# Performance work log

Hardware: AMD Instinct MI355X
Metric: run time of the kernel (lower is better)

The kernel has to match this reference:

```python
import jax, jax.numpy as jnp
import numpy as np

L = 8      # num_hidden_layers
J = 3      # num_gnn_layers
N = 2000   # num nodes (<=2000 so prune=False)
E = 32000  # num edges
R = 64     # num relations
HID = 1024 # hidden_dim
G = 128    # gnn_dim
H = 8      # num_gnn_heads
DH = G // H          # 16 per-head dim
P = 10               # pre_seq_len
KV = 8               # plm_num_kv_heads
OUT = HID // 32 * KV # out_ft_dim = 256
B = 16               # batch (h.shape[0])


def setup_inputs() -> dict:
    key = jax.random.key(0)
    ks = jax.random.split(key, 24)
    f = lambda k, s: (jax.random.normal(k, s, dtype=jnp.float32) * 0.05)
    ri = lambda k, s, hi: jax.random.randint(k, s, 0, hi, dtype=jnp.int32)
    return {
        'nft': f(ks[0], (L, N, HID)),
        'rft': f(ks[1], (L, R, HID)),
        'importances': jax.random.normal(ks[2], (N,), dtype=jnp.float32),
        'tg_w': f(ks[3], (L, HID, G)),
        'tg_b': f(ks[4], (L, G)),
        'path_w': f(ks[5], (L, J, 3 * G, G)),
        'path_b': f(ks[6], (L, J, G)),
        'attn1_w': f(ks[7], (L, J, G, H)),
        'attn2_p': f(ks[8], (L, J, H, DH)),
        'trans_w': f(ks[9], (L, G, 2 * OUT)),
        'trans_b': f(ks[10], (L, 2 * OUT)),
        'lamda': jnp.zeros((L - 1,), dtype=jnp.float32),
        'edge_src': ri(ks[11], (E,), N),
        'edge_dst': ri(ks[12], (E,), N),
        'edge_label': ri(ks[13], (E,), R),
        'h': ri(ks[14], (B,), N),
        't': ri(ks[15], (B,), N),
    }


def _gat(x, eft, src, dst, Wp, bp, Wa1, a2p):
    # x: [N, G], eft: [E, G]
    ns = x[src]                       # [E, G] gather src node feats
    ne = x[dst]                       # [E, G] gather dst node feats
    epaths = (jnp.concatenate([ns, eft, ne], axis=-1) @ Wp + bp)
    epaths = epaths.reshape(E, H, DH)           # per-edge multi-head features
    a1 = ns @ Wa1                               # [E, H]
    a2 = jnp.einsum('ehd,hd->eh', epaths, a2p)  # [E, H]
    a = jax.nn.leaky_relu(a1 + a2)              # slope 0.01, matches torch default
    # edge softmax grouped by destination node
    amax = jax.ops.segment_max(a, dst, num_segments=N)
    ex = jnp.exp(a - amax[dst])
    ssum = jax.ops.segment_sum(ex, dst, num_segments=N)
    attn = ex / ssum[dst]                       # [E, H]
    msg = epaths * attn[..., None]              # [E, H, DH]
    agg = jax.ops.segment_sum(msg, dst, num_segments=N)  # [N, H, DH]
    return jax.nn.relu(agg.reshape(N, G) + x)


def reference(nft, rft, importances, tg_w, tg_b, path_w, path_b, attn1_w,
              attn2_p, trans_w, trans_b, lamda, edge_src, edge_dst,
              edge_label, h, t):
    bsz = h.shape[0]
    # topk indices of node importances (prune=False path)
    _, imp_idx = jax.lax.top_k(importances, P)
    pkv = []
    for i in range(L):
        x = nft[i] @ tg_w[i] + tg_b[i]                       # [N, G]
        # linear-then-gather == gather-then-linear (same math, less traffic)
        rel = rft[i] @ tg_w[i] + tg_b[i]                     # [R, G]
        gnn_eft = rel[edge_label]                            # [E, G]
        for j in range(J):
            x = _gat(x, gnn_eft, edge_src, edge_dst,
                     path_w[i, j], path_b[i, j], attn1_w[i, j], attn2_p[i, j])
        past_x = x
        if i > 0:
            s = jax.nn.sigmoid(lamda[i - 1] / 0.1)
            x = s * x + (1.0 - s) * past_x   # past_x == x (as in source)
        prefix = x[imp_idx]                                  # [P, G]
        pk = jnp.tanh(prefix) @ trans_w[i] + trans_b[i]      # [P, 2*OUT]
        pk = jnp.broadcast_to(pk[None], (bsz, P, 2 * OUT))
        pk = pk.reshape(bsz, P, 2, KV, OUT // KV).transpose(2, 0, 3, 1, 4)
        pkv.append(pk)
    return jnp.stack(pkv)   # [L, 2, B, KV, P, OUT//KV]
```

## Files before the change

kernel.cpp:

```cpp
#include <hip/hip_runtime.h>
#include <hip/hip_bf16.h>
#include <math.h>

#define L_    8
#define J_    3
#define N_    2000
#define E_    32000
#define R_    64
#define HID_  1024
#define G_    128
#define H_    8
#define DH_   16
#define P_    10
#define KV_   8
#define OUT2_ 512
#define B_    16
#define ROWS_ 2064
#define CAP_  64

typedef float f32x4 __attribute__((ext_vector_type(4)));
typedef short s16x8 __attribute__((ext_vector_type(8)));

__device__ __forceinline__ void cvt_split1(float v, short& h, short& l) {
    unsigned u = __float_as_uint(v);
    h = (short)(u >> 16);
    float rem = v - __uint_as_float(u & 0xffff0000u);
    l = (short)(__float_as_uint(rem) >> 16);
}

__device__ __forceinline__ void cvt_split8(const float* v, s16x8& h, s16x8& l) {
    #pragma unroll
    for (int i = 0; i < 8; ++i) {
        unsigned u = __float_as_uint(v[i]);
        h[i] = (short)(u >> 16);
        float rem = v[i] - __uint_as_float(u & 0xffff0000u);
        l[i] = (short)(__float_as_uint(rem) >> 16);
    }
}

__device__ __forceinline__ void cvt_split8v(float4 a, float4 b, s16x8& h, s16x8& l) {
    short hh, ll;
    cvt_split1(a.x, hh, ll); h[0] = hh; l[0] = ll;
    cvt_split1(a.y, hh, ll); h[1] = hh; l[1] = ll;
    cvt_split1(a.z, hh, ll); h[2] = hh; l[2] = ll;
    cvt_split1(a.w, hh, ll); h[3] = hh; l[3] = ll;
    cvt_split1(b.x, hh, ll); h[4] = hh; l[4] = ll;
    cvt_split1(b.y, hh, ll); h[5] = hh; l[5] = ll;
    cvt_split1(b.z, hh, ll); h[6] = hh; l[6] = ll;
    cvt_split1(b.w, hh, ll); h[7] = hh; l[7] = ll;
}


__device__ __forceinline__ void place_body(int b, const int* __restrict__ dst,
                                           const int* __restrict__ src,
                                           const int* __restrict__ lab,
                                           int* __restrict__ cur,
                                           int2* __restrict__ sl) {
    int e = b * 128 + threadIdx.x;
    if (e < E_) {
        int n = dst[e];
        int slot = atomicAdd(&cur[n], 1);
        sl[n * CAP_ + slot] = make_int2(src[e], lab[e]);
    }
}

__device__ __forceinline__ void topk_body(const float* __restrict__ imp,
                                          int* __restrict__ idx_out, char* pool) {
    float* sv = (float*)pool;
    float* rv = (float*)(pool + 8192);
    int*   ri = (int*)(pool + 8704);
    int t = threadIdx.x;
    for (int i = t; i < N_; i += 128) sv[i] = imp[i];
    __syncthreads();
    for (int k = 0; k < P_; ++k) {
        float bv = -INFINITY; int bi = N_;
        for (int i = t; i < N_; i += 128) {
            float v = sv[i];
            if (v > bv || (v == bv && i < bi)) { bv = v; bi = i; }
        }
        rv[t] = bv; ri[t] = bi;
        __syncthreads();
        for (int s = 64; s > 0; s >>= 1) {
            if (t < s) {
                float v = rv[t + s]; int i2 = ri[t + s];
                if (v > rv[t] || (v == rv[t] && i2 < ri[t])) { rv[t] = v; ri[t] = i2; }
            }
            __syncthreads();
        }
        if (t == 0) { idx_out[k] = ri[0]; sv[ri[0]] = -INFINITY; }
        __syncthreads();
    }
}

__device__ __forceinline__ void psplit_body(int l, int j, int halfc, int st,
                                            const float* __restrict__ path_w,
                                            short* __restrict__ Ppk) {
    int lj = l * J_ + j;
    int col = threadIdx.x;
    int c0 = halfc ? 256 : 0;
    size_t base = (((size_t)lj * 2 + halfc) * 4 + st) * 2;
    #pragma unroll
    for (int khalf = 0; khalf < 2; ++khalf) {
        const float* src = path_w + (size_t)lj * 384 * G_
                         + (size_t)(c0 + st * 32 + khalf * 16) * G_ + col;
        short* dh = Ppk + (base + 0) * 4096 + (khalf * 128 + col) * 16;
        short* dl = Ppk + (base + 1) * 4096 + (khalf * 128 + col) * 16;
        #pragma unroll
        for (int kk = 0; kk < 16; ++kk) {
            short h, l2;
            cvt_split1(src[(size_t)kk * G_], h, l2);
            dh[kk] = h; dl[kk] = l2;
        }
    }
}

__device__ __forceinline__ void prep_body(int combo, int q,
                                          const float* __restrict__ path_w,
                                          const float* __restrict__ path_b,
                                          const float* __restrict__ attn1_w,
                                          const float* __restrict__ attn2_p,
                                          float* __restrict__ wPR,
                                          short* __restrict__ PPk,
                                          float* __restrict__ bA) {
    int j = combo / L_;
    int l = combo % L_;
    int t = threadIdx.x;
    size_t wb = (size_t)((l * J_ + j) * 384) * G_;
    size_t ob = (size_t)(j * L_ + l);
    const float* a2 = attn2_p + (size_t)(l * J_ + j) * G_;
    short* pph = PPk + (ob * 2 + 0) * 2048;
    short* ppl = PPk + (ob * 2 + 1) * 2048;
    #pragma unroll
    for (int h2 = 0; h2 < 2; ++h2) {
        int i = q * 256 + h2 * 128 + t;
        int k = i >> 3, h = i & 7;
        const float* a2h = a2 + h * DH_;
        float s1 = 0.f, s2 = 0.f, s3 = 0.f;
        for (int d = 0; d < DH_; ++d) {
            float av = a2h[d];
            int c = h * DH_ + d;
            s1 += path_w[wb + (size_t)k * G_ + c] * av;
            s3 += path_w[wb + (size_t)(128 + k) * G_ + c] * av;
            s2 += path_w[wb + (size_t)(256 + k) * G_ + c] * av;
        }
        s1 += attn1_w[((size_t)(l * J_ + j) * G_ + k) * H_ + h];
        short h1, l1, hh2, l2;
        cvt_split1(s1, h1, l1);
        cvt_split1(s2, hh2, l2);
        pph[h * 128 + k] = h1;        ppl[h * 128 + k] = l1;
        pph[(8 + h) * 128 + k] = hh2; ppl[(8 + h) * 128 + k] = l2;
        wPR[ob * H_ * G_ + h * G_ + k] = s3;
    }
    if (q == 0 && t < H_) {
        float s = 0.f;
        const float* a2h = a2 + t * DH_;
        const float* pb = path_b + (size_t)(l * J_ + j) * G_ + t * DH_;
        for (int d = 0; d < DH_; ++d) s += pb[d] * a2h[d];
        bA[ob * H_ + t] = s;
    }
}

__global__ __launch_bounds__(256) void k_pre0(
    const float* __restrict__ tg_w, short* __restrict__ WpkB,
    int* __restrict__ cur) {
    int b = blockIdx.x;
    if (b == 256) {
        for (int i = threadIdx.x; i < N_; i += 256) cur[i] = 0;
        return;
    }
    int layer = b & 7, gst = b >> 3;
    int tid = threadIdx.x;
    int col = tid & 127, khalf = tid >> 7;
    const float* src = tg_w + ((size_t)layer * HID_ + gst * 32 + khalf * 16) * G_ + col;
    short* dh = WpkB + ((size_t)(layer * 32 + gst) * 2 + 0) * 4096 + col * 32 + khalf * 16;
    short* dl = WpkB + ((size_t)(layer * 32 + gst) * 2 + 1) * 4096 + col * 32 + khalf * 16;
    #pragma unroll
    for (int kk = 0; kk < 16; ++kk) {
        short h, l;
        cvt_split1(src[(size_t)kk * G_], h, l);
        dh[kk] = h; dl[kk] = l;
    }
}

__global__ __launch_bounds__(128, 2) void k_pre3(
    const float* __restrict__ nft, const float* __restrict__ rft,
    const short* __restrict__ WpkB, const float* __restrict__ tg_b,
    float* __restrict__ x0, float* __restrict__ rel,
    const int* __restrict__ edst, const int* __restrict__ esrc,
    const int* __restrict__ elab, const float* __restrict__ imp,
    const float* __restrict__ path_w, const float* __restrict__ path_b,
    const float* __restrict__ attn1_w, const float* __restrict__ attn2_p,
    int* __restrict__ cur, int2* __restrict__ csr_sl, int* __restrict__ imp_idx,
    short* __restrict__ Ppk, float* __restrict__ wPR,
    short* __restrict__ PPk, float* __restrict__ bA) {
    __shared__ alignas(16) char POOL3[12288];
    int b = blockIdx.x;
    if (b >= 520) {
        int w = b - 520;
        if (w < 250) { place_body(w, edst, esrc, elab, cur, csr_sl); return; }
        if (w == 250) { topk_body(imp, imp_idx, POOL3); return; }
        if (w < 443) {
            int v = w - 251;
            int l = v & 7, m = v >> 3;
            int j = m % 3, hs = m / 3;
            psplit_body(l, j, hs >> 2, hs & 3, path_w, Ppk);
            return;
        }
        {
            int v = w - 443;
            prep_body(v >> 2, v & 3, path_w, path_b, attn1_w, attn2_p, wPR, PPk, bA);
            return;
        }
    }

    const int layer = b & 7;
    const int rg = b >> 3;
    const int row0 = rg * 32;
    const int tid = threadIdx.x;
    const int lane = tid & 63, wv = tid >> 6;
    const int lr = lane & 15, kg = lane >> 4;

    char* ldsb = POOL3;

    const float* gsrc0;
    const float* gsrc1;
    {
        int swz = ((lane & 7) ^ (lane >> 3)) << 2;
        int rl0 = wv * 16 + (lane >> 3);
        int rl1 = rl0 + 8;
        int g0 = row0 + rl0; if (g0 > ROWS_ - 1) g0 = ROWS_ - 1;
        int g1 = row0 + rl1; if (g1 > ROWS_ - 1) g1 = ROWS_ - 1;
        gsrc0 = ((g0 < N_) ? nft + ((size_t)layer * N_ + g0) * HID_
                           : rft + ((size_t)layer * R_ + (g0 - N_)) * HID_) + swz;
        gsrc1 = ((g1 < N_) ? nft + ((size_t)layer * N_ + g1) * HID_
                           : rft + ((size_t)layer * R_ + (g1 - N_)) * HID_) + swz;
    }
    const short* WB = WpkB + (size_t)layer * 262144 + ((wv * 64 + lr) * 32 + kg * 8);

    f32x4 zero = {0.f, 0.f, 0.f, 0.f};
    f32x4 acc[2][4];
    #pragma unroll
    for (int i = 0; i < 2; ++i)
        #pragma unroll
        for (int n = 0; n < 4; ++n) acc[i][n] = zero;

    s16x8 bs[2][4][2];

#define LDA(WR, GST) do { \
    char* lb_ = ldsb + (WR) * 4096 + wv * 2048; \
    __builtin_amdgcn_global_load_lds( \
        (const __attribute__((address_space(1))) void*)(gsrc0 + (GST) * 32), \
        (__attribute__((address_space(3))) void*)(lb_), 16, 0, 0); \
    __builtin_amdgcn_global_load_lds( \
        (const __attribute__((address_space(1))) void*)(gsrc1 + (GST) * 32), \
        (__attribute__((address_space(3))) void*)(lb_ + 1024), 16, 0, 0); \
} while (0)

#define LDB(SL, GST) do { \
    const short* bp_ = WB + (size_t)(GST) * 8192; \
    _Pragma("unroll") \
    for (int n_ = 0; n_ < 4; ++n_) { \
        bs[SL][n_][0] = *(const s16x8*)(bp_ + n_ * 512); \
        bs[SL][n_][1] = *(const s16x8*)(bp_ + n_ * 512 + 4096); \
    } \
} while (0)

#define COMP(CUR, SL) do { \
    const int o1_ = (kg * 32) ^ ((lr & 7) << 4); \
    _Pragma("unroll") \
    for (int mf_ = 0; mf_ < 2; ++mf_) { \
        const char* ap_ = ldsb + (CUR) * 4096 + (mf_ * 16 + lr) * 128; \
        float4 av0_ = *(const float4*)(ap_ + o1_); \
        float4 av1_ = *(const float4*)(ap_ + (o1_ ^ 16)); \
        s16x8 ah_, al_; \
        cvt_split8v(av0_, av1_, ah_, al_); \
        _Pragma("unroll") \
        for (int n_ = 0; n_ < 4; ++n_) { \
            acc[mf_][n_] = __builtin_amdgcn_mfma_f32_16x16x32_bf16(ah_, bs[SL][n_][0], acc[mf_][n_], 0, 0, 0); \
            acc[mf_][n_] = __builtin_amdgcn_mfma_f32_16x16x32_bf16(ah_, bs[SL][n_][1], acc[mf_][n_], 0, 0, 0); \
            acc[mf_][n_] = __builtin_amdgcn_mfma_f32_16x16x32_bf16(al_, bs[SL][n_][0], acc[mf_][n_], 0, 0, 0); \
        } \
    } \
} while (0)

#define TGITER(ST, CUR, WR, SL, SLN) do { \
    LDB(SLN, (ST) + 1); \
    LDA(WR, (ST) + 2); \
    asm volatile("s_waitcnt vmcnt(12)" ::: "memory"); \
    __builtin_amdgcn_s_barrier(); \
    COMP(CUR, SL); \
    __builtin_amdgcn_s_barrier(); \
} while (0)

    LDA(0, 0);
    LDA(1, 1);
    LDB(0, 0);
    for (int st = 0; st < 30; st += 6) {
        TGITER(st + 0, 0, 2, 0, 1);
        TGITER(st + 1, 1, 0, 1, 0);
        TGITER(st + 2, 2, 1, 0, 1);
        TGITER(st + 3, 0, 2, 1, 0);
        TGITER(st + 4, 1, 0, 0, 1);
        TGITER(st + 5, 2, 1, 1, 0);
    }
    LDB(1, 31);
    asm volatile("s_waitcnt vmcnt(10)" ::: "memory");
    __builtin_amdgcn_s_barrier();
    COMP(0, 0);
    asm volatile("s_waitcnt vmcnt(0)" ::: "memory");
    __builtin_amdgcn_s_barrier();
    COMP(1, 1);
#undef LDA
#undef LDB
#undef COMP
#undef TGITER

    #pragma unroll
    for (int n = 0; n < 4; ++n) {
        int col = wv * 64 + n * 16 + lr;
        float bias = tg_b[layer * G_ + col];
        #pragma unroll
        for (int mf = 0; mf < 2; ++mf) {
            #pragma unroll
            for (int rgi = 0; rgi < 4; ++rgi) {
                int row = row0 + mf * 16 + kg * 4 + rgi;
                if (row >= ROWS_) continue;
                float v = acc[mf][n][rgi] + bias;
                if (row < N_) x0[((size_t)layer * N_ + row) * G_ + col] = v;
                else          rel[((size_t)layer * R_ + (row - N_)) * G_ + col] = v;
            }
        }
    }
}

__device__ __forceinline__ void rel_body(
    int blk, char* pool,
    const float* __restrict__ rel, const float* __restrict__ path_w,
    const float* __restrict__ wPR, float* __restrict__ Rl, float* __restrict__ PR) {
    float (*At)[132] = (float(*)[132])pool;
    float (*Wt)[132] = (float(*)[132])(pool + 16896);
    const int tid = threadIdx.x;
    const int halfb = blk & 1;
    const int t2 = blk >> 1;
    const int l = t2 % L_;
    const int j = t2 / L_;
    const int row0 = halfb * 32;
    const size_t ob = (size_t)(j * L_ + l);
    {
        int ar = tid >> 3, aq2 = tid & 7;
        const float* asrc = rel + ((size_t)l * R_ + row0 + ar) * G_ + aq2 * 16;
        float4 a0 = ((const float4*)asrc)[0], a1 = ((const float4*)asrc)[1];
        float4 a2 = ((const float4*)asrc)[2], a3 = ((const float4*)asrc)[3];
        *(float4*)&At[ar][aq2 * 16]      = a0;
        *(float4*)&At[ar][aq2 * 16 + 4]  = a1;
        *(float4*)&At[ar][aq2 * 16 + 8]  = a2;
        *(float4*)&At[ar][aq2 * 16 + 12] = a3;
    }
    const size_t wb = (size_t)((l * J_ + j) * 384) * G_;
    const int wrow = tid >> 3, wq = tid & 7;
    float4 rW0, rW1, rW2, rW3;
    auto loadW = [&](int kt) {
        const float* src = path_w + wb + (size_t)(128 + kt * 32 + wrow) * G_ + wq * 16;
        rW0 = ((const float4*)src)[0]; rW1 = ((const float4*)src)[1];
        rW2 = ((const float4*)src)[2]; rW3 = ((const float4*)src)[3];
    };
    const int tr = tid >> 4;
    const int tc = tid & 15;
    float4 acc[2][2];
    acc[0][0] = make_float4(0, 0, 0, 0); acc[0][1] = make_float4(0, 0, 0, 0);
    acc[1][0] = make_float4(0, 0, 0, 0); acc[1][1] = make_float4(0, 0, 0, 0);
    loadW(0);
    for (int wt = 0; wt < 4; ++wt) {
        __syncthreads();
        *(float4*)&Wt[wrow][wq * 16]      = rW0;
        *(float4*)&Wt[wrow][wq * 16 + 4]  = rW1;
        *(float4*)&Wt[wrow][wq * 16 + 8]  = rW2;
        *(float4*)&Wt[wrow][wq * 16 + 12] = rW3;
        __syncthreads();
        if (wt + 1 < 4) loadW(wt + 1);
        #pragma unroll
        for (int kk = 0; kk < 32; ++kk) {
            float4 w0 = *(const float4*)&Wt[kk][tc * 4];
            float4 w1 = *(const float4*)&Wt[kk][64 + tc * 4];
            float a0 = At[tr * 2][wt * 32 + kk];
            float a1 = At[tr * 2 + 1][wt * 32 + kk];
            acc[0][0].x += a0 * w0.x; acc[0][0].y += a0 * w0.y;
            acc[0][0].z += a0 * w0.z; acc[0][0].w += a0 * w0.w;
            acc[0][1].x += a0 * w1.x; acc[0][1].y += a0 * w1.y;
            acc[0][1].z += a0 * w1.z; acc[0][1].w += a0 * w1.w;
            acc[1][0].x += a1 * w0.x; acc[1][0].y += a1 * w0.y;
            acc[1][0].z += a1 * w0.z; acc[1][0].w += a1 * w0.w;
            acc[1][1].x += a1 * w1.x; acc[1][1].y += a1 * w1.y;
            acc[1][1].z += a1 * w1.z; acc[1][1].w += a1 * w1.w;
        }
    }
    #pragma unroll
    for (int r2 = 0; r2 < 2; ++r2) {
        int row = row0 + tr * 2 + r2;
        float* dst = Rl + (ob * R_ + row) * G_;
        *(float4*)(dst + tc * 4) = acc[r2][0];
        *(float4*)(dst + 64 + tc * 4) = acc[r2][1];
    }
    {
        int prow = tid >> 3, ph = tid & 7;
        const float* wp = wPR + (ob * H_ + ph) * G_;
        float s = 0.f;
        for (int k = 0; k < G_; ++k) s += At[prow][k] * wp[k];
        PR[(ob * R_ + row0 + prow) * H_ + ph] = s;
    }
}

__global__ __launch_bounds__(256) void k_proj2(
    const float* __restrict__ xcur, const short* __restrict__ Ppk,
    const short* __restrict__ PPkj, const float* __restrict__ bAj,
    const float* __restrict__ path_b, int j,
    float* __restrict__ Xs, float* __restrict__ XdB,
    float* __restrict__ PS, float* __restrict__ PDb,
    const float* __restrict__ rel, const float* __restrict__ path_w,
    const float* __restrict__ wPR, float* __restrict__ Rl, float* __restrict__ PR) {
    __shared__ alignas(16) char POOL[39424];
    if (blockIdx.x >= 512) { rel_body(blockIdx.x - 512, POOL, rel, path_w, wPR, Rl, PR); return; }
    short (*Ah)[40]   = (short(*)[40])(POOL);
    short (*Al)[40]   = (short(*)[40])(POOL + 5120);
    short (*Wh)[40]   = (short(*)[40])(POOL + 10240);
    short (*Wl)[40]   = (short(*)[40])(POOL + 20480);
    short (*PPh)[136] = (short(*)[136])(POOL + 30720);
    short (*PPl)[136] = (short(*)[136])(POOL + 35072);
    const int tid = threadIdx.x;
    const int layer = blockIdx.x & 7;
    const int rest = blockIdx.x >> 3;
    const int halfb = rest & 1;
    const int rg = rest >> 1;
    const int row0 = rg * 64;

    const int arow = tid >> 2, aq = tid & 3;
    int gra = row0 + arow; if (gra >= N_) gra = N_ - 1;
    const float* asrc = xcur + ((size_t)layer * N_ + gra) * G_;
    const int wcol = tid & 127, wkh = tid >> 7;

    const int lane = tid & 63, wv = tid >> 6;
    const int lr = lane & 15, lk = (lane >> 4) * 8;

    if (!halfb) {
        int col = tid >> 4, koff = (tid & 15) * 8;
        s16x8 vh = *(const s16x8*)(PPkj + ((size_t)layer * 2 + 0) * 2048 + tid * 8);
        s16x8 vl = *(const s16x8*)(PPkj + ((size_t)layer * 2 + 1) * 2048 + tid * 8);
        *(s16x8*)&PPh[col][koff] = vh;
        *(s16x8*)&PPl[col][koff] = vl;
    }

    f32x4 zero = {0.f, 0.f, 0.f, 0.f};
    f32x4 acc[4][2];
    f32x4 acc_pp[2];
    #pragma unroll
    for (int i = 0; i < 4; ++i) { acc[i][0] = zero; acc[i][1] = zero; }
    acc_pp[0] = zero; acc_pp[1] = zero;

    float aa[8];
    s16x8 wh0, wh1, wl0, wl1;
    const size_t pbase = (((size_t)(layer * J_ + j) * 2 + halfb) * 4) * 2;
    auto ldG = [&](int st) {
        int kk0 = st * 32;
        *(float4*)&aa[0] = *(const float4*)(asrc + kk0 + aq * 8);
        *(float4*)&aa[4] = *(const float4*)(asrc + kk0 + aq * 8 + 4);
        const s16x8* ph = (const s16x8*)(Ppk + (pbase + (size_t)st * 2 + 0) * 4096 + tid * 16);
        const s16x8* pl = (const s16x8*)(Ppk + (pbase + (size_t)st * 2 + 1) * 4096 + tid * 16);
        wh0 = ph[0]; wh1 = ph[1];
        wl0 = pl[0]; wl1 = pl[1];
    };
    ldG(0);
    for (int st = 0; st < 4; ++st) {
        __syncthreads();
        {
            s16x8 h, l; cvt_split8(aa, h, l);
            *(s16x8*)&Ah[arow][aq * 8] = h;
            *(s16x8*)&Al[arow][aq * 8] = l;
            *(s16x8*)&Wh[wcol][wkh * 16]     = wh0;
            *(s16x8*)&Wh[wcol][wkh * 16 + 8] = wh1;
            *(s16x8*)&Wl[wcol][wkh * 16]     = wl0;
            *(s16x8*)&Wl[wcol][wkh * 16 + 8] = wl1;
        }
        __syncthreads();
        if (st + 1 < 4) ldG(st + 1);
        s16x8 bh[2], bl[2];
        #pragma unroll
        for (int c = 0; c < 2; ++c) {
            int col = wv * 32 + c * 16 + lr;
            bh[c] = *(s16x8*)&Wh[col][lk];
            bl[c] = *(s16x8*)&Wl[col][lk];
        }
        s16x8 ppb_h, ppb_l;
        if (!halfb) {
            ppb_h = *(s16x8*)&PPh[lr][st * 32 + lk];
            ppb_l = *(s16x8*)&PPl[lr][st * 32 + lk];
        }
        #pragma unroll
        for (int mf = 0; mf < 4; ++mf) {
            s16x8 ah = *(s16x8*)&Ah[mf * 16 + lr][lk];
            s16x8 al = *(s16x8*)&Al[mf * 16 + lr][lk];
            #pragma unroll
            for (int c = 0; c < 2; ++c) {
                acc[mf][c] = __builtin_amdgcn_mfma_f32_16x16x32_bf16(ah, bh[c], acc[mf][c], 0, 0, 0);
                acc[mf][c] = __builtin_amdgcn_mfma_f32_16x16x32_bf16(ah, bl[c], acc[mf][c], 0, 0, 0);
                acc[mf][c] = __builtin_amdgcn_mfma_f32_16x16x32_bf16(al, bh[c], acc[mf][c], 0, 0, 0);
            }
            if (!halfb && (mf >> 1) == wv) {
                int i = mf & 1;
                acc_pp[i] = __builtin_amdgcn_mfma_f32_16x16x32_bf16(ah, ppb_h, acc_pp[i], 0, 0, 0);
                acc_pp[i] = __builtin_amdgcn_mfma_f32_16x16x32_bf16(ah, ppb_l, acc_pp[i], 0, 0, 0);
                acc_pp[i] = __builtin_amdgcn_mfma_f32_16x16x32_bf16(al, ppb_h, acc_pp[i], 0, 0, 0);
            }
        }
    }
    const float* pb = path_b + (size_t)(layer * J_ + j) * G_;
    float* outp = halfb ? XdB : Xs;
    const int rbase = (lane >> 4) * 4;
    #pragma unroll
    for (int mf = 0; mf < 4; ++mf) {
        #pragma unroll
        for (int c = 0; c < 2; ++c) {
            int col = wv * 32 + c * 16 + lr;
            float bias = halfb ? pb[col] : 0.f;
            #pragma unroll
            for (int rgi = 0; rgi < 4; ++rgi) {
                int row = row0 + mf * 16 + rbase + rgi;
                if (row < N_) outp[((size_t)layer * N_ + row) * G_ + col] = acc[mf][c][rgi] + bias;
            }
        }
    }
    if (!halfb) {
        #pragma unroll
        for (int i = 0; i < 2; ++i) {
            int mf = wv * 2 + i;
            #pragma unroll
            for (int rgi = 0; rgi < 4; ++rgi) {
                int row = row0 + mf * 16 + rbase + rgi;
                if (row >= N_) continue;
                float val = acc_pp[i][rgi];
                if (lr < 8) PS[((size_t)layer * N_ + row) * H_ + lr] = val;
                else        PDb[((size_t)layer * N_ + row) * H_ + (lr - 8)] = val + bAj[layer * H_ + (lr - 8)];
            }
        }
    }
}

__global__ __launch_bounds__(256) void k_node(
    const float* __restrict__ xcur, const float* __restrict__ Xs,
    const float* __restrict__ XdB, const float* __restrict__ Rlj,
    const float* __restrict__ PS, const float* __restrict__ PDb,
    const float* __restrict__ PRj,
    const int* __restrict__ cnt, const int2* __restrict__ csr_sl,
    float* __restrict__ xnext) {
    int l = blockIdx.x & 7;
    int n = (blockIdx.x >> 3) * 4 + (threadIdx.x >> 6);
    int lane = threadIdx.x & 63;
    int o0 = n * CAP_, o1 = o0 + cnt[n];
    const float* xr = xcur + ((size_t)l * N_ + n) * G_;
    float xv0 = xr[lane], xv1 = xr[lane + 64];
    float xd0 = XdB[((size_t)l * N_ + n) * G_ + lane];
    float xd1 = XdB[((size_t)l * N_ + n) * G_ + lane + 64];
    float out0, out1;
    if (o1 == o0) {
        out0 = fmaxf(xv0, 0.f);
        out1 = fmaxf(xv1, 0.f);
    } else {
        const int h0 = lane >> 4, h1 = h0 + 4;
        const float pd0 = PDb[((size_t)l * N_ + n) * H_ + h0];
        const float pd1 = PDb[((size_t)l * N_ + n) * H_ + h1];
        const float* PSl = PS + (size_t)l * N_ * H_;
        const float* PRl = PRj + (size_t)l * R_ * H_;
        const float* Xsl = Xs + (size_t)l * N_ * G_;
        const float* Rll = Rlj + (size_t)l * R_ * G_;
        float acc0 = 0.f, acc1 = 0.f, sum0 = 0.f, sum1 = 0.f;
        #pragma unroll 2
        for (int k = o0; k < o1; ++k) {
            int2 sl = csr_sl[k];
            float lg0 = PSl[sl.x * H_ + h0] + PRl[sl.y * H_ + h0] + pd0;
            float lg1 = PSl[sl.x * H_ + h1] + PRl[sl.y * H_ + h1] + pd1;
            lg0 = (lg0 >= 0.f) ? lg0 : 0.01f * lg0;
            lg1 = (lg1 >= 0.f) ? lg1 : 0.01f * lg1;
            float e0 = __expf(lg0), e1 = __expf(lg1);
            float v0 = Xsl[(size_t)sl.x * G_ + lane]      + Rll[(size_t)sl.y * G_ + lane];
            float v1 = Xsl[(size_t)sl.x * G_ + lane + 64] + Rll[(size_t)sl.y * G_ + lane + 64];
            acc0 += e0 * v0; sum0 += e0;
            acc1 += e1 * v1; sum1 += e1;
        }
        out0 = fmaxf(acc0 / sum0 + xd0 + xv0, 0.f);
        out1 = fmaxf(acc1 / sum1 + xd1 + xv1, 0.f);
    }
    float* dst = xnext + ((size_t)l * N_ + n) * G_;
    dst[lane] = out0;
    dst[lane + 64] = out1;
}

__global__ __launch_bounds__(256) void k_out(
    const float* __restrict__ xfin, const int* __restrict__ imp_idx,
    const float* __restrict__ trans_w, const float* __restrict__ trans_b,
    float* __restrict__ out) {
    int blk = blockIdx.x;
    int layer = blk / (P_ * 2);
    int rem = blk % (P_ * 2);
    int p = rem >> 1;
    int half = rem & 1;
    __shared__ float th[G_];
    int t = threadIdx.x;
    int row = imp_idx[p];
    if (t < G_) th[t] = tanhf(xfin[((size_t)layer * N_ + row) * G_ + t]);
    __syncthreads();
    int c = half * 256 + t;
    float s = trans_b[layer * OUT2_ + c];
    const float* W = trans_w + (size_t)layer * G_ * OUT2_ + c;
    #pragma unroll 4
    for (int k = 0; k < G_; ++k) s += th[k] * W[(size_t)k * OUT2_];
    int c2 = c >> 8, kv = (c >> 5) & 7, oo = c & 31;
    for (int b = 0; b < B_; ++b) {
        out[(((((size_t)layer * 2 + c2) * B_ + b) * KV_ + kv) * P_ + p) * 32 + oo] = s;
    }
}

extern "C" void kernel_launch(void* const* d_in, const int* in_sizes, int n_in,
                              void* d_out, int out_size, void* d_ws, size_t ws_size,
                              hipStream_t stream) {
    const float* nft     = (const float*)d_in[0];
    const float* rft     = (const float*)d_in[1];
    const float* imp     = (const float*)d_in[2];
    const float* tg_w    = (const float*)d_in[3];
    const float* tg_b    = (const float*)d_in[4];
    const float* path_w  = (const float*)d_in[5];
    const float* path_b  = (const float*)d_in[6];
    const float* attn1_w = (const float*)d_in[7];
    const float* attn2_p = (const float*)d_in[8];
    const float* trans_w = (const float*)d_in[9];
    const float* trans_b = (const float*)d_in[10];
    const int* esrc = (const int*)d_in[12];
    const int* edst = (const int*)d_in[13];
    const int* elab = (const int*)d_in[14];
    float* out = (float*)d_out;

    char* w = (char*)d_ws;
    size_t off = 0;
    auto alloc = [&](size_t bytes) {
        void* p = w + off;
        off += (bytes + 255) & ~(size_t)255;
        return p;
    };
    float* x0      = (float*)alloc((size_t)L_ * N_ * G_ * 4);
    float* x1      = (float*)alloc((size_t)L_ * N_ * G_ * 4);
    float* rel     = (float*)alloc((size_t)L_ * R_ * G_ * 4);
    float* Xs      = (float*)alloc((size_t)L_ * N_ * G_ * 4);
    float* XdB     = (float*)alloc((size_t)L_ * N_ * G_ * 4);
    float* Rl      = (float*)alloc((size_t)J_ * L_ * R_ * G_ * 4);
    float* PS      = (float*)alloc((size_t)L_ * N_ * H_ * 4);
    float* PDb     = (float*)alloc((size_t)L_ * N_ * H_ * 4);
    float* PR      = (float*)alloc((size_t)J_ * L_ * R_ * H_ * 4);
    float* wPR     = (float*)alloc((size_t)J_ * L_ * H_ * G_ * 4);
    float* bA      = (float*)alloc((size_t)J_ * L_ * H_ * 4);
    short* Wpk     = (short*)alloc((size_t)L_ * 32 * 2 * 4096 * 2);
    short* Ppk     = (short*)alloc((size_t)L_ * J_ * 2 * 4 * 2 * 4096 * 2);
    short* PPk     = (short*)alloc((size_t)J_ * L_ * 2 * 2048 * 2);
    int*   cur     = (int*)alloc(N_ * 4);
    int2*  csr_sl  = (int2*)alloc((size_t)N_ * CAP_ * 8);
    int*   imp_idx = (int*)alloc(P_ * 4);

    k_pre0<<<257, 256, 0, stream>>>(tg_w, Wpk, cur);
    k_pre3<<<520 + 250 + 1 + 192 + 96, 128, 0, stream>>>(
        nft, rft, Wpk, tg_b, x0, rel,
        edst, esrc, elab, imp, path_w, path_b, attn1_w, attn2_p,
        cur, csr_sl, imp_idx, Ppk, wPR, PPk, bA);

    float* xc = x0;
    float* xn = x1;
    for (int j = 0; j < J_; ++j) {
        int grid = (j == 0) ? (512 + J_ * L_ * 2) : 512;
        k_proj2<<<grid, 256, 0, stream>>>(
            xc, Ppk, PPk + (size_t)j * L_ * 2 * 2048, bA + (size_t)j * L_ * H_,
            path_b, j, Xs, XdB, PS, PDb,
            rel, path_w, wPR, Rl, PR);
        k_node<<<L_ * 500, 256, 0, stream>>>(
            xc, Xs, XdB, Rl + (size_t)j * L_ * R_ * G_, PS, PDb,
            PR + (size_t)j * L_ * R_ * H_,
            cur, csr_sl, xn);
        float* tmp = xc; xc = xn; xn = tmp;
    }
    k_out<<<L_ * P_ * 2, 256, 0, stream>>>(xc, imp_idx, trans_w, trans_b, out);
}
```

Before: 182.3 us.

## Halve row tile of node-feature GEMM to double block count

Each block of the pre-projection GEMM now covers 16 rows instead of 32, so the grid grows from 520 to 1032 tiles. Each block issues a single A-row load per stage, keeps one accumulator set, and uses half the LDS. Launch bounds rise to allow more resident blocks, and the vmcnt waits are retuned to the smaller load count. The aim is more parallelism and better latency hiding on this memory-bound stage. In exchange, every B-weight fragment is now loaded twice as often across blocks, since each block reuses it over fewer rows.

```diff
diff --git a/kernel.cpp b/kernel.cpp
--- a/kernel.cpp
+++ b/kernel.cpp
@@ -17,6 +17,7 @@
 #define B_    16
 #define ROWS_ 2064
 #define CAP_  64
+#define GB_   1032
 
 typedef float f32x4 __attribute__((ext_vector_type(4)));
 typedef short s16x8 __attribute__((ext_vector_type(8)));
@@ -182,7 +183,7 @@
     }
 }
 
-__global__ __launch_bounds__(128, 2) void k_pre3(
+__global__ __launch_bounds__(128, 4) void k_pre3(
     const float* __restrict__ nft, const float* __restrict__ rft,
     const short* __restrict__ WpkB, const float* __restrict__ tg_b,
     float* __restrict__ x0, float* __restrict__ rel,
@@ -195,8 +196,8 @@
     short* __restrict__ PPk, float* __restrict__ bA) {
     __shared__ alignas(16) char POOL3[12288];
     int b = blockIdx.x;
-    if (b >= 520) {
-        int w = b - 520;
+    if (b >= GB_) {
+        int w = b - GB_;
         if (w < 250) { place_body(w, edst, esrc, elab, cur, csr_sl); return; }
         if (w == 250) { topk_body(imp, imp_idx, POOL3); return; }
         if (w < 443) {
@@ -215,7 +216,7 @@
 
     const int layer = b & 7;
     const int rg = b >> 3;
-    const int row0 = rg * 32;
+    const int row0 = rg * 16;
     const int tid = threadIdx.x;
     const int lane = tid & 63, wv = tid >> 6;
     const int lr = lane & 15, kg = lane >> 4;
@@ -223,37 +224,27 @@
     char* ldsb = POOL3;
 
     const float* gsrc0;
-    const float* gsrc1;
     {
         int swz = ((lane & 7) ^ (lane >> 3)) << 2;
-        int rl0 = wv * 16 + (lane >> 3);
-        int rl1 = rl0 + 8;
-        int g0 = row0 + rl0; if (g0 > ROWS_ - 1) g0 = ROWS_ - 1;
-        int g1 = row0 + rl1; if (g1 > ROWS_ - 1) g1 = ROWS_ - 1;
-        gsrc0 = ((g0 < N_) ? nft + ((size_t)layer * N_ + g0) * HID_
-                           : rft + ((size_t)layer * R_ + (g0 - N_)) * HID_) + swz;
-        gsrc1 = ((g1 < N_) ? nft + ((size_t)layer * N_ + g1) * HID_
-                           : rft + ((size_t)layer * R_ + (g1 - N_)) * HID_) + swz;
+        int rb = row0 + wv * 8 + (lane >> 3);
+        if (rb > ROWS_ - 1) rb = ROWS_ - 1;
+        gsrc0 = ((rb < N_) ? nft + ((size_t)layer * N_ + rb) * HID_
+                           : rft + ((size_t)layer * R_ + (rb - N_)) * HID_) + swz;
     }
     const short* WB = WpkB + (size_t)layer * 262144 + ((wv * 64 + lr) * 32 + kg * 8);
 
     f32x4 zero = {0.f, 0.f, 0.f, 0.f};
-    f32x4 acc[2][4];
-    #pragma unroll
-    for (int i = 0; i < 2; ++i)
-        #pragma unroll
-        for (int n = 0; n < 4; ++n) acc[i][n] = zero;
+    f32x4 acc4[4];
+    #pragma unroll
+    for (int n = 0; n < 4; ++n) acc4[n] = zero;
 
     s16x8 bs[2][4][2];
 
 #define LDA(WR, GST) do { \
-    char* lb_ = ldsb + (WR) * 4096 + wv * 2048; \
+    char* lb_ = ldsb + (WR) * 2048 + wv * 1024; \
     __builtin_amdgcn_global_load_lds( \
         (const __attribute__((address_space(1))) void*)(gsrc0 + (GST) * 32), \
         (__attribute__((address_space(3))) void*)(lb_), 16, 0, 0); \
-    __builtin_amdgcn_global_load_lds( \
-        (const __attribute__((address_space(1))) void*)(gsrc1 + (GST) * 32), \
-        (__attribute__((address_space(3))) void*)(lb_ + 1024), 16, 0, 0); \
 } while (0)
 
 #define LDB(SL, GST) do { \
@@ -267,26 +258,23 @@
 
 #define COMP(CUR, SL) do { \
     const int o1_ = (kg * 32) ^ ((lr & 7) << 4); \
+    const char* ap_ = ldsb + (CUR) * 2048 + lr * 128; \
+    float4 av0_ = *(const float4*)(ap_ + o1_); \
+    float4 av1_ = *(const float4*)(ap_ + (o1_ ^ 16)); \
+    s16x8 ah_, al_; \
+    cvt_split8v(av0_, av1_, ah_, al_); \
     _Pragma("unroll") \
-    for (int mf_ = 0; mf_ < 2; ++mf_) { \
-        const char* ap_ = ldsb + (CUR) * 4096 + (mf_ * 16 + lr) * 128; \
-        float4 av0_ = *(const float4*)(ap_ + o1_); \
-        float4 av1_ = *(const float4*)(ap_ + (o1_ ^ 16)); \
-        s16x8 ah_, al_; \
-        cvt_split8v(av0_, av1_, ah_, al_); \
-        _Pragma("unroll") \
-        for (int n_ = 0; n_ < 4; ++n_) { \
-            acc[mf_][n_] = __builtin_amdgcn_mfma_f32_16x16x32_bf16(ah_, bs[SL][n_][0], acc[mf_][n_], 0, 0, 0); \
-            acc[mf_][n_] = __builtin_amdgcn_mfma_f32_16x16x32_bf16(ah_, bs[SL][n_][1], acc[mf_][n_], 0, 0, 0); \
-            acc[mf_][n_] = __builtin_amdgcn_mfma_f32_16x16x32_bf16(al_, bs[SL][n_][0], acc[mf_][n_], 0, 0, 0); \
-        } \
+    for (int n_ = 0; n_ < 4; ++n_) { \
+        acc4[n_] = __builtin_amdgcn_mfma_f32_16x16x32_bf16(ah_, bs[SL][n_][0], acc4[n_], 0, 0, 0); \
+        acc4[n_] = __builtin_amdgcn_mfma_f32_16x16x32_bf16(ah_, bs[SL][n_][1], acc4[n_], 0, 0, 0); \
+        acc4[n_] = __builtin_amdgcn_mfma_f32_16x16x32_bf16(al_, bs[SL][n_][0], acc4[n_], 0, 0, 0); \
     } \
 } while (0)
 
 #define TGITER(ST, CUR, WR, SL, SLN) do { \
     LDB(SLN, (ST) + 1); \
     LDA(WR, (ST) + 2); \
-    asm volatile("s_waitcnt vmcnt(12)" ::: "memory"); \
+    asm volatile("s_waitcnt vmcnt(9)" ::: "memory"); \
     __builtin_amdgcn_s_barrier(); \
     COMP(CUR, SL); \
     __builtin_amdgcn_s_barrier(); \
@@ -304,7 +292,7 @@
         TGITER(st + 5, 2, 1, 1, 0);
     }
     LDB(1, 31);
-    asm volatile("s_waitcnt vmcnt(10)" ::: "memory");
+    asm volatile("s_waitcnt vmcnt(9)" ::: "memory");
     __builtin_amdgcn_s_barrier();
     COMP(0, 0);
     asm volatile("s_waitcnt vmcnt(0)" ::: "memory");
@@ -320,15 +308,12 @@
         int col = wv * 64 + n * 16 + lr;
         float bias = tg_b[layer * G_ + col];
         #pragma unroll
-        for (int mf = 0; mf < 2; ++mf) {
-            #pragma unroll
-            for (int rgi = 0; rgi < 4; ++rgi) {
-                int row = row0 + mf * 16 + kg * 4 + rgi;
-                if (row >= ROWS_) continue;
-                float v = acc[mf][n][rgi] + bias;
-                if (row < N_) x0[((size_t)layer * N_ + row) * G_ + col] = v;
-                else          rel[((size_t)layer * R_ + (row - N_)) * G_ + col] = v;
-            }
+        for (int rgi = 0; rgi < 4; ++rgi) {
+            int row = row0 + kg * 4 + rgi;
+            if (row >= ROWS_) continue;
+            float v = acc4[n][rgi] + bias;
+            if (row < N_) x0[((size_t)layer * N_ + row) * G_ + col] = v;
+            else          rel[((size_t)layer * R_ + (row - N_)) * G_ + col] = v;
         }
     }
 }
@@ -663,7 +648,7 @@
     int*   imp_idx = (int*)alloc(P_ * 4);
 
     k_pre0<<<257, 256, 0, stream>>>(tg_w, Wpk, cur);
-    k_pre3<<<520 + 250 + 1 + 192 + 96, 128, 0, stream>>>(
+    k_pre3<<<GB_ + 250 + 1 + 192 + 96, 128, 0, stream>>>(
         nft, rft, Wpk, tg_b, x0, rel,
         edst, esrc, elab, imp, path_w, path_b, attn1_w, attn2_p,
         cur, csr_sl, imp_idx, Ppk, wPR, PPk, bA);
```

Result: slower. 191.4 us (+5.0%).
